# Optimization experiments

Hardware: AMD Instinct MI355X
Metric: run time of the kernel (lower is better)

Reference implementation:

```python
import jax, jax.numpy as jnp
import numpy as np

IN_F = 4096
OUT_F = 11008
GROUP_SIZE = 128
NUM_GROUPS = (IN_F + GROUP_SIZE - 1) // GROUP_SIZE  # 32
N_HIGH = int(OUT_F * 0.25)   # 2752
N_LOW = OUT_F - N_HIGH       # 8256
B, S = 2, 2048


def setup_inputs() -> dict:
    key = jax.random.key(0)
    ks = jax.random.split(key, 9)
    x = jax.random.normal(ks[0], (B, S, IN_F), dtype=jnp.float32)
    # INT8 symmetric codes for high-precision columns
    high_prec_weight = jax.random.randint(ks[1], (IN_F, N_HIGH), -128, 128, dtype=jnp.int32)
    # per-group, per-column scales (positive, realistic magnitude)
    high_prec_scales = jax.random.uniform(ks[2], (NUM_GROUPS, N_HIGH), jnp.float32, 1e-4, 2e-2)
    # 4-bit asymmetric codes in [0, 15]
    low_prec_weight = jax.random.randint(ks[3], (IN_F, N_LOW), 0, 16, dtype=jnp.int32)
    low_prec_scales = jax.random.uniform(ks[4], (IN_F, 1), jnp.float32, 1e-4, 2e-2)
    low_prec_scales2 = jax.random.uniform(ks[5], (1, N_LOW), jnp.float32, 0.5, 2.0)
    low_prec_zeros = jnp.round(jax.random.uniform(ks[6], (IN_F, 1), jnp.float32, 0.0, 15.0))
    # inverse column permutation restoring original order
    col_indices_inv = jax.random.permutation(ks[7], OUT_F).astype(jnp.int64)
    bias = jax.random.normal(ks[8], (OUT_F,), dtype=jnp.float32) * 0.02
    return {
        "x": x,
        "high_prec_weight": high_prec_weight,
        "high_prec_scales": high_prec_scales,
        "low_prec_weight": low_prec_weight,
        "low_prec_scales": low_prec_scales,
        "low_prec_scales2": low_prec_scales2,
        "low_prec_zeros": low_prec_zeros,
        "col_indices_inv": col_indices_inv,
        "bias": bias,
    }


def _dequantize(high_w, high_scales, low_w, low_s1, low_s2, low_z, col_inv):
    # High: group-wise symmetric INT8 dequant. K divisible by GROUP_SIZE here (no pad).
    w_high = (high_w.astype(jnp.float32)
              .reshape(NUM_GROUPS, GROUP_SIZE, N_HIGH)
              * high_scales[:, None, :]).reshape(IN_F, N_HIGH)
    # Low: SINQ dual-scale asymmetric dequant: ((q - z) * s1) * s2
    w_low = (low_w.astype(jnp.float32) - low_z) * low_s1 * low_s2
    # Reassemble original column order: W_kn [in_features, out_features]
    w = jnp.concatenate([w_high, w_low], axis=1)[:, col_inv]
    return w


def reference(x, high_prec_weight, high_prec_scales, low_prec_weight,
              low_prec_scales, low_prec_scales2, low_prec_zeros,
              col_indices_inv, bias):
    w_kn = _dequantize(high_prec_weight, high_prec_scales, low_prec_weight,
                       low_prec_scales, low_prec_scales2, low_prec_zeros,
                       col_indices_inv)
    # F.linear(x, W_original) with W_original = w_kn.T  ->  x @ w_kn
    out = jnp.einsum('bsk,kn->bsn', x, w_kn) + bias
    return out
```

## Files before the change

kernel.cpp:

```cpp
#include <hip/hip_runtime.h>
#include <hip/hip_bf16.h>

#define IN_F   4096
#define OUT_F  11008
#define NHIGH  2752
#define NLOW   8256
#define M_TOT  4096

typedef __attribute__((ext_vector_type(8))) short bf16x8;
typedef __attribute__((ext_vector_type(4))) float f32x4;
typedef __attribute__((ext_vector_type(4))) float f32x4v;

__device__ __forceinline__ short f2bf(float f) {
    union { float f; unsigned u; } v; v.f = f;
    unsigned r = (v.u + 0x7fffu + ((v.u >> 16) & 1u)) >> 16;
    return (short)(r & 0xffffu);
}

__device__ __forceinline__ void async16(const void* g, const void* l) {
    __builtin_amdgcn_global_load_lds(
        (const __attribute__((address_space(1))) unsigned int*)g,
        (__attribute__((address_space(3))) unsigned int*)l, 16, 0, 0);
}

__global__ void fwd_perm_kernel(const int* __restrict__ cinv, int* __restrict__ fwd) {
    int n = blockIdx.x * blockDim.x + threadIdx.x;
    if (n < OUT_F) fwd[cinv[n]] = n;
}

__global__ void cvt_x_kernel(const float* __restrict__ x, short* __restrict__ xb) {
    const int nv = (M_TOT * IN_F) / 8;
    for (int i = blockIdx.x * blockDim.x + threadIdx.x; i < nv;
         i += gridDim.x * blockDim.x) {
        const f32x4v* p = (const f32x4v*)(x + (long)i * 8);
        f32x4v a = __builtin_nontemporal_load(p);
        f32x4v b = __builtin_nontemporal_load(p + 1);
        bf16x8 o;
        o[0] = f2bf(a[0]); o[1] = f2bf(a[1]); o[2] = f2bf(a[2]); o[3] = f2bf(a[3]);
        o[4] = f2bf(b[0]); o[5] = f2bf(b[1]); o[6] = f2bf(b[2]); o[7] = f2bf(b[3]);
        *(bf16x8*)(xb + (long)i * 8) = o;
    }
}

__global__ void dequant_kernel(const int* __restrict__ hw, const float* __restrict__ hs,
                               const int* __restrict__ lw, const float* __restrict__ s1,
                               const float* __restrict__ s2, const float* __restrict__ zp,
                               const int* __restrict__ fwd,
                               short* __restrict__ wt) {
    __shared__ short tile[64 * 66];
    const int t  = threadIdx.x;
    const int c0 = blockIdx.x * 64;
    const int k0 = blockIdx.y * 64;
    const int cl = t & 63;
    const int w  = t >> 6;

    if (c0 < NHIGH) {
        const int ci = c0 + cl;
        #pragma unroll
        for (int i = 0; i < 16; ++i) {
            const int kl = w + 4 * i;
            const int k  = k0 + kl;
            int   q   = __builtin_nontemporal_load(&hw[(long)k * NHIGH + ci]);
            float val = (float)q * hs[(k >> 7) * NHIGH + ci];
            tile[cl * 66 + kl] = f2bf(val);
        }
    } else {
        const int ci = c0 - NHIGH + cl;
        const float s2v = s2[ci];
        #pragma unroll
        for (int i = 0; i < 16; ++i) {
            const int kl = w + 4 * i;
            const int k  = k0 + kl;
            int   q   = __builtin_nontemporal_load(&lw[(long)k * NLOW + ci]);
            float val = ((float)q - zp[k]) * s1[k] * s2v;
            tile[cl * 66 + kl] = f2bf(val);
        }
    }
    __syncthreads();
    const int oc = t >> 2;
    const int kq = (t & 3) * 16;
    bf16x8 o0, o1;
    #pragma unroll
    for (int j = 0; j < 8; ++j) {
        o0[j] = tile[oc * 66 + kq + j];
        o1[j] = tile[oc * 66 + kq + 8 + j];
    }
    const int ndst = fwd[c0 + oc];
    short* dst = wt + (long)ndst * IN_F + k0 + kq;
    *(bf16x8*)dst       = o0;
    *(bf16x8*)(dst + 8) = o1;
}

#define BM 256
#define BN 256
#define BK 64
#define KT (IN_F / BK)
#define NTIL (OUT_F / BN)
#define MTIL (M_TOT / BM)
#define NWG2 (NTIL * MTIL)

#define BAR()    __builtin_amdgcn_s_barrier()
#define LGKM0()  asm volatile("s_waitcnt lgkmcnt(0)" ::: "memory")
#define VMC(N)   asm volatile("s_waitcnt vmcnt(" #N ")" ::: "memory")

__global__ __launch_bounds__(512, 2) void gemm_kernel(
    const short* __restrict__ A,
    const short* __restrict__ Bt,
    const float* __restrict__ bias,
    float* __restrict__ C) {
    __shared__ __align__(16) short lds_s[65536];
    char* const lds = (char*)lds_s;

    const int t    = threadIdx.x;
    const int lane = t & 63;
    const int w    = t >> 6;
    const int wr   = w >> 2;
    const int wc   = w & 3;

    const int swz = (blockIdx.x % 8) * (NWG2 / 8) + blockIdx.x / 8;
    const int mb  = swz / NTIL;
    const int nb  = swz % NTIL;
    const int m0  = mb * BM;
    const int n0  = nb * BN;

    const int srow = w * 8 + (lane >> 3);
    const int scb  = ((lane & 7) ^ (lane >> 3)) * 16;
    const char* gA0 = (const char*)A  + (long)(m0 + srow) * (IN_F * 2) + scb;
    const char* gB0 = (const char*)Bt + (long)(n0 + srow) * (IN_F * 2) + scb;

    const int rl  = (lane & 15) * 128;
    const int kb0 = ((lane >> 4) * 16) ^ ((lane & 7) << 4);
    const int kb1 = kb0 ^ 64;

#define STAGE(gbase, region_off, h, ktile) do {                                  \
        const char* _g = (gbase) + (long)((h) * 128) * (IN_F * 2) + (ktile) * 128; \
        char* _l = lds + (region_off) + (h) * 16384 + w * 1024;                  \
        async16(_g,                        _l);                                  \
        async16(_g + (long)64 * (IN_F * 2), _l + 8192);                          \
    } while (0)

    f32x4 acc[8][4];
    #pragma unroll
    for (int i = 0; i < 8; ++i)
        #pragma unroll
        for (int j = 0; j < 4; ++j)
            acc[i][j] = (f32x4){0.f, 0.f, 0.f, 0.f};

    bf16x8 a[4][2], b0[2][2], b1[2][2];

#define RD_A(buf, mq) do {                                                       \
        char* _p = lds + (buf) * 65536 + wr * 16384 + (mq) * 8192 + rl;          \
        _Pragma("unroll")                                                        \
        for (int _j = 0; _j < 4; ++_j) {                                         \
            a[_j][0] = *(const bf16x8*)(_p + _j * 2048 + kb0);                   \
            a[_j][1] = *(const bf16x8*)(_p + _j * 2048 + kb1);                   \
        }                                                                        \
    } while (0)

#define RD_B(buf, nq, breg) do {                                                 \
        char* _p = lds + (buf) * 65536 + 32768 + wc * 8192 + (nq) * 4096 + rl;   \
        _Pragma("unroll")                                                        \
        for (int _n = 0; _n < 2; ++_n) {                                         \
            breg[_n][0] = *(const bf16x8*)(_p + _n * 2048 + kb0);                \
            breg[_n][1] = *(const bf16x8*)(_p + _n * 2048 + kb1);                \
        }                                                                        \
    } while (0)

#define MMA_Q(mq, nq, breg) do {                                                 \
        __builtin_amdgcn_s_setprio(1);                                           \
        _Pragma("unroll")                                                        \
        for (int _j = 0; _j < 4; ++_j)                                           \
        _Pragma("unroll")                                                        \
        for (int _n = 0; _n < 2; ++_n) {                                         \
            acc[(mq)*4+_j][(nq)*2+_n] = __builtin_amdgcn_mfma_f32_16x16x32_bf16( \
                a[_j][0], breg[_n][0], acc[(mq)*4+_j][(nq)*2+_n], 0, 0, 0);      \
            acc[(mq)*4+_j][(nq)*2+_n] = __builtin_amdgcn_mfma_f32_16x16x32_bf16( \
                a[_j][1], breg[_n][1], acc[(mq)*4+_j][(nq)*2+_n], 0, 0, 0);      \
        }                                                                        \
        __builtin_amdgcn_s_setprio(0);                                           \
    } while (0)

    STAGE(gA0, 0,     0, 0);
    STAGE(gA0, 0,     1, 0);
    STAGE(gB0, 32768, 0, 0);
    STAGE(gB0, 32768, 1, 0);
    STAGE(gA0, 65536, 0, 1);
    VMC(2);
    BAR();

    #pragma unroll 1
    for (int it = 0; it < KT / 2; ++it) {
        const int kt1 = 2 * it + 1;
        const int kt2 = (2 * it + 2 < KT) ? 2 * it + 2 : KT - 1;
        const int kt3 = (2 * it + 3 < KT) ? 2 * it + 3 : KT - 1;

        RD_A(0, 0); RD_B(0, 0, b0);
        STAGE(gA0, 65536 + 0,     1, kt1);
        BAR(); LGKM0();
        MMA_Q(0, 0, b0);
        BAR();

        RD_B(0, 1, b1);
        STAGE(gB0, 65536 + 32768, 0, kt1);
        BAR(); LGKM0();
        MMA_Q(0, 1, b1);
        BAR();

        RD_A(0, 1);
        STAGE(gB0, 65536 + 32768, 1, kt1);
        BAR(); LGKM0();
        MMA_Q(1, 1, b1);
        BAR();

        STAGE(gA0, 0,             0, kt2);
        BAR();
        MMA_Q(1, 0, b0);
        VMC(2);
        BAR();

        RD_A(1, 0); RD_B(1, 0, b0);
        STAGE(gA0, 0,             1, kt2);
        BAR(); LGKM0();
        MMA_Q(0, 0, b0);
        BAR();

        RD_B(1, 1, b1);
        STAGE(gB0, 32768,         0, kt2);
        BAR(); LGKM0();
        MMA_Q(0, 1, b1);
        BAR();

        RD_A(1, 1);
        STAGE(gB0, 32768,         1, kt2);
        BAR(); LGKM0();
        MMA_Q(1, 1, b1);
        BAR();

        STAGE(gA0, 65536,         0, kt3);
        BAR();
        MMA_Q(1, 0, b0);
        VMC(2);
        BAR();
    }

    asm volatile("s_waitcnt vmcnt(0)" ::: "memory");

    const int er = m0 + wr * 128 + (lane >> 4) * 4;
    const int ec = n0 + wc * 64 + (lane & 15);
    #pragma unroll
    for (int ni = 0; ni < 4; ++ni) {
        const float bv = bias[ec + ni * 16];
        #pragma unroll
        for (int mi = 0; mi < 8; ++mi) {
            #pragma unroll
            for (int r = 0; r < 4; ++r) {
                __builtin_nontemporal_store(
                    acc[mi][ni][r] + bv,
                    &C[(long)(er + mi * 16 + r) * OUT_F + ec + ni * 16]);
            }
        }
    }
}

extern "C" void kernel_launch(void* const* d_in, const int* in_sizes, int n_in,
                              void* d_out, int out_size, void* d_ws, size_t ws_size,
                              hipStream_t stream) {
    const float* x    = (const float*)d_in[0];
    const int*   hw   = (const int*)d_in[1];
    const float* hs   = (const float*)d_in[2];
    const int*   lw   = (const int*)d_in[3];
    const float* s1   = (const float*)d_in[4];
    const float* s2   = (const float*)d_in[5];
    const float* zp   = (const float*)d_in[6];
    const int*   cinv = (const int*)d_in[7];
    const float* bias = (const float*)d_in[8];
    float*       out  = (float*)d_out;

    short* wt  = (short*)d_ws;
    short* xb  = (short*)((char*)d_ws + (size_t)OUT_F * IN_F * 2);
    int*   fwd = (int*)((char*)d_ws + (size_t)OUT_F * IN_F * 2
                                    + (size_t)M_TOT * IN_F * 2);

    fwd_perm_kernel<<<(OUT_F + 255) / 256, 256, 0, stream>>>(cinv, fwd);
    cvt_x_kernel<<<2048, 256, 0, stream>>>(x, xb);
    dequant_kernel<<<dim3(OUT_F / 64, IN_F / 64), 256, 0, stream>>>(
        hw, hs, lw, s1, s2, zp, fwd, wt);
    gemm_kernel<<<NWG2, 512, 0, stream>>>(xb, wt, bias, out);
}
```

Before: 404.0 us.

## Replace phased LDS pipeline with simple double-buffer and regroup tile swizzle

```diff
diff --git a/kernel.cpp b/kernel.cpp
--- a/kernel.cpp
+++ b/kernel.cpp
@@ -100,8 +100,7 @@
 #define NWG2 (NTIL * MTIL)
 
 #define BAR()    __builtin_amdgcn_s_barrier()
-#define LGKM0()  asm volatile("s_waitcnt lgkmcnt(0)" ::: "memory")
-#define VMC(N)   asm volatile("s_waitcnt vmcnt(" #N ")" ::: "memory")
+#define VMC0()   asm volatile("s_waitcnt vmcnt(0)" ::: "memory")
 
 __global__ __launch_bounds__(512, 2) void gemm_kernel(
     const short* __restrict__ A,
@@ -117,11 +116,13 @@
     const int wr   = w >> 2;
     const int wc   = w & 3;
 
-    const int swz = (blockIdx.x % 8) * (NWG2 / 8) + blockIdx.x / 8;
-    const int mb  = swz / NTIL;
-    const int nb  = swz % NTIL;
-    const int m0  = mb * BM;
-    const int n0  = nb * BN;
+    const int swz   = (blockIdx.x % 8) * (NWG2 / 8) + blockIdx.x / 8;
+    const int sr    = swz / (4 * NTIL);
+    const int in_sr = swz % (4 * NTIL);
+    const int nb    = in_sr / 4;
+    const int mb    = sr * 4 + (in_sr & 3);
+    const int m0    = mb * BM;
+    const int n0    = nb * BN;
 
     const int srow = w * 8 + (lane >> 3);
     const int scb  = ((lane & 7) ^ (lane >> 3)) * 16;
@@ -146,14 +147,14 @@
         for (int j = 0; j < 4; ++j)
             acc[i][j] = (f32x4){0.f, 0.f, 0.f, 0.f};
 
-    bf16x8 a[4][2], b0[2][2], b1[2][2];
-
-#define RD_A(buf, mq) do {                                                       \
+    bf16x8 aA[4][2], aB[4][2], b0[2][2], b1[2][2];
+
+#define RD_A(buf, mq, areg) do {                                                 \
         char* _p = lds + (buf) * 65536 + wr * 16384 + (mq) * 8192 + rl;          \
         _Pragma("unroll")                                                        \
         for (int _j = 0; _j < 4; ++_j) {                                         \
-            a[_j][0] = *(const bf16x8*)(_p + _j * 2048 + kb0);                   \
-            a[_j][1] = *(const bf16x8*)(_p + _j * 2048 + kb1);                   \
+            areg[_j][0] = *(const bf16x8*)(_p + _j * 2048 + kb0);                \
+            areg[_j][1] = *(const bf16x8*)(_p + _j * 2048 + kb1);                \
         }                                                                        \
     } while (0)
 
@@ -166,84 +167,50 @@
         }                                                                        \
     } while (0)
 
-#define MMA_Q(mq, nq, breg) do {                                                 \
+#define MMA_Q(mq, nq, areg, breg) do {                                           \
         __builtin_amdgcn_s_setprio(1);                                           \
         _Pragma("unroll")                                                        \
         for (int _j = 0; _j < 4; ++_j)                                           \
         _Pragma("unroll")                                                        \
         for (int _n = 0; _n < 2; ++_n) {                                         \
             acc[(mq)*4+_j][(nq)*2+_n] = __builtin_amdgcn_mfma_f32_16x16x32_bf16( \
-                a[_j][0], breg[_n][0], acc[(mq)*4+_j][(nq)*2+_n], 0, 0, 0);      \
+                areg[_j][0], breg[_n][0], acc[(mq)*4+_j][(nq)*2+_n], 0, 0, 0);   \
             acc[(mq)*4+_j][(nq)*2+_n] = __builtin_amdgcn_mfma_f32_16x16x32_bf16( \
-                a[_j][1], breg[_n][1], acc[(mq)*4+_j][(nq)*2+_n], 0, 0, 0);      \
+                areg[_j][1], breg[_n][1], acc[(mq)*4+_j][(nq)*2+_n], 0, 0, 0);   \
         }                                                                        \
         __builtin_amdgcn_s_setprio(0);                                           \
+    } while (0)
+
+#define TILE_BODY(buf, ktn) do {                                                 \
+        RD_A(buf, 0, aA);                                                        \
+        RD_B(buf, 0, b0);                                                        \
+        RD_B(buf, 1, b1);                                                        \
+        RD_A(buf, 1, aB);                                                        \
+        STAGE(gA0, ((buf)^1) * 65536,         0, ktn);                           \
+        STAGE(gA0, ((buf)^1) * 65536,         1, ktn);                           \
+        STAGE(gB0, ((buf)^1) * 65536 + 32768, 0, ktn);                           \
+        STAGE(gB0, ((buf)^1) * 65536 + 32768, 1, ktn);                           \
+        MMA_Q(0, 0, aA, b0);                                                     \
+        MMA_Q(0, 1, aA, b1);                                                     \
+        MMA_Q(1, 1, aB, b1);                                                     \
+        MMA_Q(1, 0, aB, b0);                                                     \
+        VMC0(); BAR();                                                           \
     } while (0)
 
     STAGE(gA0, 0,     0, 0);
     STAGE(gA0, 0,     1, 0);
     STAGE(gB0, 32768, 0, 0);
     STAGE(gB0, 32768, 1, 0);
-    STAGE(gA0, 65536, 0, 1);
-    VMC(2);
+    VMC0();
     BAR();
 
     #pragma unroll 1
     for (int it = 0; it < KT / 2; ++it) {
         const int kt1 = 2 * it + 1;
         const int kt2 = (2 * it + 2 < KT) ? 2 * it + 2 : KT - 1;
-        const int kt3 = (2 * it + 3 < KT) ? 2 * it + 3 : KT - 1;
-
-        RD_A(0, 0); RD_B(0, 0, b0);
-        STAGE(gA0, 65536 + 0,     1, kt1);
-        BAR(); LGKM0();
-        MMA_Q(0, 0, b0);
-        BAR();
-
-        RD_B(0, 1, b1);
-        STAGE(gB0, 65536 + 32768, 0, kt1);
-        BAR(); LGKM0();
-        MMA_Q(0, 1, b1);
-        BAR();
-
-        RD_A(0, 1);
-        STAGE(gB0, 65536 + 32768, 1, kt1);
-        BAR(); LGKM0();
-        MMA_Q(1, 1, b1);
-        BAR();
-
-        STAGE(gA0, 0,             0, kt2);
-        BAR();
-        MMA_Q(1, 0, b0);
-        VMC(2);
-        BAR();
-
-        RD_A(1, 0); RD_B(1, 0, b0);
-        STAGE(gA0, 0,             1, kt2);
-        BAR(); LGKM0();
-        MMA_Q(0, 0, b0);
-        BAR();
-
-        RD_B(1, 1, b1);
-        STAGE(gB0, 32768,         0, kt2);
-        BAR(); LGKM0();
-        MMA_Q(0, 1, b1);
-        BAR();
-
-        RD_A(1, 1);
-        STAGE(gB0, 32768,         1, kt2);
-        BAR(); LGKM0();
-        MMA_Q(1, 1, b1);
-        BAR();
-
-        STAGE(gA0, 65536,         0, kt3);
-        BAR();
-        MMA_Q(1, 0, b0);
-        VMC(2);
-        BAR();
-    }
-
-    asm volatile("s_waitcnt vmcnt(0)" ::: "memory");
+        TILE_BODY(0, kt1);
+        TILE_BODY(1, kt2);
+    }
 
     const int er = m0 + wr * 128 + (lane >> 4) * 4;
     const int ec = n0 + wc * 64 + (lane & 15);
```

Result: faster. 393.3 us (median of 2 runs) (-2.6%).
